# Kernel optimization log

Hardware: AMD Instinct MI355X
Metric: run time of the kernel (lower is better)

The kernel has to match this reference:

```python
import jax, jax.numpy as jnp
import numpy as np

B, S, DIN, H, N, L_S4, L_RES, ED = 512, 500, 14, 128, 256, 4, 6, 256


def setup_inputs() -> dict:
    key = jax.random.key(0)
    ks = jax.random.split(key, 32)
    f = jnp.float32
    rn = lambda k, sh, s: jax.random.normal(k, sh, f) * s
    inp = {
        'x': rn(ks[0], (B, S, DIN), 1.0),
        'timesteps': jax.random.randint(ks[1], (B,), 0, 1000),
        'mask': (jax.random.uniform(ks[2], (B, S, 1)) < 0.9).astype(f),
        'observed': rn(ks[3], (B, S, DIN), 1.0),
        'W_in': rn(ks[4], (DIN, H), DIN ** -0.5), 'b_in': jnp.zeros((H,), f),
        'time_W1': rn(ks[5], (ED, 2 * H), ED ** -0.5), 'time_b1': jnp.zeros((2 * H,), f),
        'time_W2': rn(ks[6], (2 * H, H), (2 * H) ** -0.5), 'time_b2': jnp.zeros((H,), f),
        's4_ln_g': jnp.ones((L_S4, H), f), 's4_ln_b': jnp.zeros((L_S4, H), f),
        's4_logA': jnp.log(0.5 * jnp.ones((L_S4, H, N), f)),
        's4_Aim': jnp.broadcast_to(np.pi * jnp.arange(N, dtype=f), (L_S4, H, N)).copy(),
        's4_Cre': rn(ks[7], (L_S4, H, N), 0.5 ** 0.5),
        's4_Cim': rn(ks[8], (L_S4, H, N), 0.5 ** 0.5),
        's4_D': rn(ks[9], (L_S4, H), 1.0),
        's4_logdt': jax.random.uniform(ks[10], (L_S4, H), f, np.log(0.001), np.log(0.1)),
        's4_Wo': rn(ks[11], (L_S4, H, H), H ** -0.5), 's4_bo': jnp.zeros((L_S4, H), f),
        'res_ln_g': jnp.ones((L_RES, H), f), 'res_ln_b': jnp.zeros((L_RES, H), f),
        'res_W1': rn(ks[12], (L_RES, H, 2 * H), H ** -0.5), 'res_b1': jnp.zeros((L_RES, 2 * H), f),
        'res_W2': rn(ks[13], (L_RES, 2 * H, H), (2 * H) ** -0.5), 'res_b2': jnp.zeros((L_RES, H), f),
        'W_out': rn(ks[14], (H, DIN), H ** -0.5), 'b_out': jnp.zeros((DIN,), f),
    }
    return inp


def _ln(x, g, b):
    m = x.mean(-1, keepdims=True)
    v = ((x - m) ** 2).mean(-1, keepdims=True)
    return (x - m) * jax.lax.rsqrt(v + 1e-5) * g + b


def reference(x, timesteps, mask, observed, W_in, b_in, time_W1, time_b1, time_W2,
              time_b2, s4_ln_g, s4_ln_b, s4_logA, s4_Aim, s4_Cre, s4_Cim, s4_D,
              s4_logdt, s4_Wo, s4_bo, res_ln_g, res_ln_b, res_W1, res_b1, res_W2,
              res_b2, W_out, b_out):
    Bb, Ss, _ = x.shape
    Hh = W_in.shape[1]
    x_cond = x * mask + observed
    # sinusoidal positional encoding gated by mask -> [B,S,H]
    pos = jnp.arange(Ss, dtype=jnp.float32)
    div = jnp.exp(-jnp.log(10000.0) * 2.0 * jnp.arange(Hh // 2, dtype=jnp.float32) / Hh)
    ang = pos[:, None] * div
    pe = jnp.concatenate([jnp.sin(ang), jnp.cos(ang)], -1)  # [S,H]
    h = x_cond @ W_in + b_in + pe[None] * mask
    # S4D layers: prenorm -> FFT causal conv with Vandermonde kernel -> GELU -> proj -> residual
    t_idx = jnp.arange(Ss, dtype=jnp.float32)
    for l in range(s4_logA.shape[0]):
        z = _ln(h, s4_ln_g[l], s4_ln_b[l])
        dt = jnp.exp(s4_logdt[l])[:, None]                       # [H,1]
        A = -jnp.exp(s4_logA[l]) + 1j * s4_Aim[l]                # [H,N]
        dtA = dt * A
        C = (s4_Cre[l] + 1j * s4_Cim[l]) * (jnp.exp(dtA) - 1.0) / A
        V = jnp.exp(dtA[:, :, None] * t_idx)                     # [H,N,S]
        K = 2.0 * jnp.einsum('hn,hnl->hl', C, V).real            # [H,S]
        u = jnp.transpose(z, (0, 2, 1))                          # [B,H,S]
        n = 2 * Ss
        y = jnp.fft.irfft(jnp.fft.rfft(u, n) * jnp.fft.rfft(K, n), n)[..., :Ss]
        y = y + s4_D[l][None, :, None] * u
        y = jax.nn.gelu(jnp.transpose(y, (0, 2, 1)), approximate=False)
        h = h + y @ s4_Wo[l] + s4_bo[l]
    # diffusion time embedding
    half = time_W1.shape[0] // 2
    emb = jnp.log(10000.0) / (half - 1)
    freqs = jnp.exp(-emb * jnp.arange(half, dtype=jnp.float32))
    te = timesteps.astype(jnp.float32)[:, None] * freqs
    te = jnp.concatenate([jnp.sin(te), jnp.cos(te)], -1)
    te = jax.nn.silu(te @ time_W1 + time_b1) @ time_W2 + time_b2
    h = h + te[:, None, :]
    # residual MLP blocks
    for l in range(res_W1.shape[0]):
        z = _ln(h, res_ln_g[l], res_ln_b[l])
        h = h + jax.nn.gelu(z @ res_W1[l] + res_b1[l], approximate=False) @ res_W2[l] + res_b2[l]
    return h @ W_out + b_out
```

## Files before the change

### kernel.cpp

```cpp
#include <hip/hip_runtime.h>
#include <math.h>

#define B_ 512
#define S_ 500
#define SP_ 512
#define DIN_ 14
#define H_ 128
#define N_ 256
#define NT_ 256000

#define SWZ(r) ((((r) ^ ((r) >> 4)) & 15) << 4)

typedef __attribute__((ext_vector_type(8))) short short8v;
typedef __attribute__((ext_vector_type(4))) short short4v;
typedef __attribute__((ext_vector_type(4))) float f32x4;

__device__ __forceinline__ float gelu_f(float x) {
    float e = __expf(-1.702f * x);
    return __fdividef(x, 1.0f + e);
}
__device__ __forceinline__ short f2bf(float f) {
    unsigned u = __builtin_bit_cast(unsigned, f);
    u += 0x7fffu + ((u >> 16) & 1u);
    return (short)(u >> 16);
}
__device__ __forceinline__ float bf2f(short s) {
    return __builtin_bit_cast(float, ((unsigned)(unsigned short)s) << 16);
}

__global__ __launch_bounds__(256) void k_kmat(
    const float* __restrict__ logA, const float* __restrict__ Aim,
    const float* __restrict__ Cre, const float* __restrict__ Cim,
    const float* __restrict__ logdt, float* __restrict__ Km)
{
    int lh = blockIdx.x;
    __shared__ float sCr[256], sCi[256], sAr[256], sAif[256];
    {
        int n = threadIdx.x;
        int idx = lh * N_ + n;
        double dt  = exp((double)logdt[lh]);
        double Are = -exp((double)logA[idx]);
        double Aiv = (double)Aim[idx];
        double ar  = dt * Are, ai = dt * Aiv;
        double er  = exp(ar);
        double E1r = er * cos(ai) - 1.0, E1i = er * sin(ai);
        double inv = 1.0 / (Are * Are + Aiv * Aiv);
        double qR  = (E1r * Are + E1i * Aiv) * inv;
        double qI  = (E1i * Are - E1r * Aiv) * inv;
        double cre = (double)Cre[idx], cim = (double)Cim[idx];
        sCr[n] = (float)(cre * qR - cim * qI);
        sCi[n] = (float)(cre * qI + cim * qR);
        sAr[n] = (float)ar;
        sAif[n] = (float)fmod(ai, 6.283185307179586476925286766559);
    }
    __syncthreads();
    for (int s = threadIdx.x; s < SP_; s += 256) {
        float acc = 0.0f;
        if (s < S_) {
            float fs = (float)s;
            for (int n = 0; n < N_; ++n) {
                float er = __expf(sAr[n] * fs);
                float y = sAif[n] * fs;
                y -= 6.28318530717958648f * rintf(y * 0.159154943091895336f);
                float sn, cs; __sincosf(y, &sn, &cs);
// ... 51 lines not shown
        float m = mask[tok];
        float a0 = b0, a1 = b1;
        const float* xp = x + (size_t)tok * DIN_;
        const float* op = obs + (size_t)tok * DIN_;
#pragma unroll
        for (int d = 0; d < DIN_; ++d) {
            float xc = xp[d] * m + op[d];
            a0 += xc * w0[d];
            a1 += xc * w1[d];
        }
        float h0 = a0 + pet[s * 128 + lane] * m;
        float h1 = a1 + pet[s * 128 + lane + 64] * m;
        float s1 = h0 + h1, s2 = h0 * h0 + h1 * h1;
#pragma unroll
        for (int off = 32; off > 0; off >>= 1) {
            s1 += __shfl_xor(s1, off, 64);
            s2 += __shfl_xor(s2, off, 64);
        }
        float mu = s1 * 0.0078125f;
        float rs = rsqrtf(s2 * 0.0078125f - mu * mu + 1e-5f);
        if (lane == 0) st[tok] = make_float2(mu, rs);
        h[(size_t)tok * H_ + lane] = h0;
        h[(size_t)tok * H_ + lane + 64] = h1;
    }
}

__global__ __launch_bounds__(256) void k_temb(
    const int* __restrict__ ts, const float* __restrict__ W1,
    const float* __restrict__ b1, const float* __restrict__ W2,
    const float* __restrict__ b2, float* __restrict__ te)
{
    __shared__ float feat[256];
    __shared__ float mid[256];
    int b = blockIdx.x, j = threadIdx.x;
    float t = (float)ts[b];
    float fr = expf(-0.07252236513367075f * (float)(j & 127));
    float ang = t * fr;
    feat[j] = (j < 128) ? sinf(ang) : cosf(ang);
    __syncthreads();
    float acc = b1[j];
    for (int k = 0; k < 256; ++k) acc += feat[k] * W1[k * 256 + j];
    mid[j] = acc / (1.0f + expf(-acc));
    __syncthreads();
    if (j < 128) {
        float a2 = b2[j];
        for (int k = 0; k < 256; ++k) a2 += mid[k] * W2[k * 128 + j];
        te[b * 128 + j] = a2;
    }
}

__global__ __launch_bounds__(256) void k_wcast(
    const float* __restrict__ Wo, const float* __restrict__ rW1,
    const float* __restrict__ rW2,
    short* __restrict__ WoT, short* __restrict__ W1T, short* __restrict__ W2T)
{
    int i = blockIdx.x * 256 + threadIdx.x;
    if (i < 65536) {
        int l = i >> 14, r = i & 16383, n = r >> 7, k = r & 127;
        WoT[i] = f2bf(Wo[(size_t)(l * 128 + k) * 128 + n]);
    } else if (i < 262144) {
        int j = i - 65536;
        int l = j >> 15, r = j & 32767, n = r >> 7, k = r & 127;
        W1T[j] = f2bf(rW1[(size_t)(l * 128 + k) * 256 + n]);
    } else if (i < 458752) {
        int j = i - 262144;
        int l = j >> 15, r = j & 32767, n = r >> 8, k = r & 255;
        W2T[j] = f2bf(rW2[(size_t)(l * 256 + k) * 128 + n]);
    }
}

__global__ __launch_bounds__(256) void k_ln_tb(
    const float* __restrict__ h, const float2* __restrict__ stc,
    const float* __restrict__ g, const float* __restrict__ be,
    short* __restrict__ ubt)
{
    int b = blockIdx.x, s0 = blockIdx.y * 64;
    int ntok = min(64, S_ - s0);
    __shared__ float tile[64 * 129];
    __shared__ float mu_[64], rs_[64];
    for (int idx = threadIdx.x; idx < (ntok << 7); idx += 256) {
        int i = idx >> 7, k = idx & 127;
        tile[i * 129 + k] = h[(size_t)(b * S_ + s0 + i) * H_ + k];
    }
    if (threadIdx.x < ntok) {
        float2 ms = stc[(size_t)b * S_ + s0 + threadIdx.x];
        mu_[threadIdx.x] = ms.x; rs_[threadIdx.x] = ms.y;
    }
    __syncthreads();
    for (int idx = threadIdx.x; idx < 128 * 32; idx += 256) {
        int k = idx >> 5, i = (idx & 31) * 2;
        float v0 = (i < ntok)     ? (tile[i * 129 + k]       - mu_[i])     * rs_[i]     * g[k] + be[k] : 0.f;
        float v1 = (i + 1 < ntok) ? (tile[(i + 1) * 129 + k] - mu_[i + 1]) * rs_[i + 1] * g[k] + be[k] : 0.f;
        unsigned lo = (unsigned short)f2bf(v0);
        unsigned hi = (unsigned short)f2bf(v1);
        *(unsigned*)(ubt + ((size_t)b * H_ + k) * SP_ + s0 + i) = lo | (hi << 16);
    }
}

__global__ __launch_bounds__(256) void k_cgemm(
    const short* __restrict__ ubt, const short* __restrict__ Tblk,
    const float* __restrict__ D, short* __restrict__ ybt)
{
    __shared__ short As[16384];
    __shared__ short Bs[16384];
    int hh = blockIdx.x, si = blockIdx.y, bt = blockIdx.z;
    int tid = threadIdx.x;
    int lane = tid & 63, wid = tid >> 6;
    int wm = wid >> 1, wn = wid & 1;
    int fr = lane & 15, ko = (lane >> 4) << 3;
    const short* Ab = ubt + ((size_t)(bt * 128) * H_ + hh) * SP_;

    f32x4 acc[4][4];
    f32x4 zv = {0.f, 0.f, 0.f, 0.f};
#pragma unroll
    for (int m = 0; m < 4; ++m)
#pragma unroll
        for (int n = 0; n < 4; ++n) acc[m][n] = zv;

    for (int tj = 0; tj <= si; ++tj) {
        if (tj) __syncthreads();
// ... 143 lines not shown
                }
                acc[m][n][j] = v;
                s1 += v; s2 += v * v;
            }
            s1 += __shfl_xor(s1, 1, 64); s2 += __shfl_xor(s2, 1, 64);
            s1 += __shfl_xor(s1, 2, 64); s2 += __shfl_xor(s2, 2, 64);
            s1 += __shfl_xor(s1, 4, 64); s2 += __shfl_xor(s2, 4, 64);
            s1 += __shfl_xor(s1, 8, 64); s2 += __shfl_xor(s2, 8, 64);
            if (fr == 0) {
                red[(wn * 128 + rl) * 2]     = s1;
                red[(wn * 128 + rl) * 2 + 1] = s2;
            }
        }
    }
    __syncthreads();
#pragma unroll
    for (int m = 0; m < 4; ++m) {
#pragma unroll
        for (int j = 0; j < 4; ++j) {
            int rl = wm * 64 + m * 16 + (lane >> 4) * 4 + j;
            int R = bm * 128 + rl;
            int b_ = R >> 9, s = R & 511;
            bool valid = (s < S_);
            float s1 = red[rl * 2]     + red[(128 + rl) * 2];
            float s2 = red[rl * 2 + 1] + red[(128 + rl) * 2 + 1];
            float mu = s1 * 0.0078125f;
            float rs = rsqrtf(s2 * 0.0078125f - mu * mu + 1e-5f);
            if (valid && fr == 0 && wn == 0)
                st[(size_t)b_ * S_ + s] = make_float2(mu, rs);
            if (un) {
#pragma unroll
                for (int n = 0; n < 4; ++n) {
                    int C = wn * 64 + n * 16 + fr;
                    float z = valid ? (acc[m][n][j] - mu) * rs * gn[C] + bn[C] : 0.f;
                    *(short*)((char*)znT + C * 256 + ((rl * 2) ^ SWZ(C))) = f2bf(z);
                }
            }
        }
    }
    if (un) {
        __syncthreads();
#pragma unroll
        for (int p = 0; p < 8; ++p) {
            int idx = p * 256 + tid;
            int C = idx >> 4, rlg = idx & 15;
            short8v z8 = *(const short8v*)((const char*)znT + C * 256 + ((rlg * 16) ^ SWZ(C)));
            *(short8v*)(un + (((size_t)(bl * 128 + C)) << 9) + s0t + rlg * 8) = z8;
        }
    }
}

__global__ __launch_bounds__(512) void k_mlp(
    float* hres, const float2* __restrict__ st,
    const short* __restrict__ W1T, const float* __restrict__ rb1,
    const short* __restrict__ W2T, const float* __restrict__ rb2,
    const float* __restrict__ g6, const float* __restrict__ b6)
{
    __shared__ __align__(16) char As1[32768];
    __shared__ __align__(16) char BsA[32768];
    int tid = threadIdx.x;
    int lane = tid & 63, wid = tid >> 6;
    int tq = wid >> 1, cq = wid & 1;
    int fr = lane & 15, q = lane >> 4;
    int ko = q * 8, q4 = q * 4;
    size_t tok0 = (size_t)blockIdx.x * 128;

    f32x4 v[4][2];
    f32x4 zvv = {0.f, 0.f, 0.f, 0.f};

#pragma unroll
    for (int nn = 0; nn < 2; ++nn) {
        int tok = tq * 32 + nn * 16 + fr;
        float2 ms = st[tok0 + tok];
        const float* hp = hres + (tok0 + tok) * 128;
#pragma unroll
        for (int m2 = 0; m2 < 4; ++m2) {
            int cb = m2 * 32 + cq * 16 + q4;
            float4 hv = *(const float4*)(hp + cb);
            v[m2][nn][0] = hv.x; v[m2][nn][1] = hv.y;
            v[m2][nn][2] = hv.z; v[m2][nn][3] = hv.w;
            float4 gv = *(const float4*)(g6 + cb);
            float4 bv = *(const float4*)(b6 + cb);
            short4v z;
            z[0] = f2bf((hv.x - ms.x) * ms.y * gv.x + bv.x);
            z[1] = f2bf((hv.y - ms.x) * ms.y * gv.y + bv.y);
            z[2] = f2bf((hv.z - ms.x) * ms.y * gv.z + bv.z);
            z[3] = f2bf((hv.w - ms.x) * ms.y * gv.w + bv.w);
            *(short4v*)(As1 + tok * 256 + ((cb * 2) ^ SWZ(tok))) = z;
        }
    }

    for (int l = 0; l < 6; ++l) {
        const short* W1 = W1T + l * 32768;
        const short* W2 = W2T + l * 32768;

        f32x4 acc1[2][4][2];
#pragma unroll
        for (int gy = 0; gy < 2; ++gy)
#pragma unroll
            for (int m1 = 0; m1 < 4; ++m1)
#pragma unroll
                for (int nn = 0; nn < 2; ++nn) acc1[gy][m1][nn] = zvv;

#pragma unroll
        for (int gy = 0; gy < 2; ++gy) {
#pragma unroll
            for (int p = 0; p < 4; ++p) {
                int idx = p * 512 + tid;
                int row = idx >> 4, c16 = idx & 15;
                int byt = row * 256 + ((c16 * 16) ^ SWZ(row));
                *(short8v*)(BsA + byt) =
                    *(const short8v*)(W1 + (size_t)(gy * 128 + row) * 128 + c16 * 8);
            }
            __syncthreads();
#pragma unroll
            for (int ks = 0; ks < 4; ++ks) {
                short8v b[2];
#pragma unroll
                for (int nn = 0; nn < 2; ++nn) {
                    int row = tq * 32 + nn * 16 + fr;
                    b[nn] = *(const short8v*)(As1 + row * 256 + (((ks * 32 + ko) * 2) ^ SWZ(row)));
                }
#pragma unroll
                for (int m1 = 0; m1 < 4; ++m1) {
                    int row = m1 * 32 + cq * 16 + fr;
                    short8v a = *(const short8v*)(BsA + row * 256 + (((ks * 32 + ko) * 2) ^ SWZ(row)));
#pragma unroll
                    for (int nn = 0; nn < 2; ++nn)
                        acc1[gy][m1][nn] = __builtin_amdgcn_mfma_f32_16x16x32_bf16(
                            a, b[nn], acc1[gy][m1][nn], 0, 0, 0);
                }
            }
            __syncthreads();
        }

        f32x4 acc2[4][2];
#pragma unroll
        for (int m2 = 0; m2 < 4; ++m2)
#pragma unroll
            for (int nn = 0; nn < 2; ++nn) acc2[m2][nn] = zvv;
#pragma unroll
        for (int kk = 0; kk < 2; ++kk) {
#pragma unroll
            for (int m1 = 0; m1 < 4; ++m1) {
                int nb = m1 * 32 + cq * 16 + q4;
                float4 bv = *(const float4*)(rb1 + l * 256 + kk * 128 + nb);
#pragma unroll
                for (int nn = 0; nn < 2; ++nn) {
                    int tok = tq * 32 + nn * 16 + fr;
                    short4v mz;
                    mz[0] = f2bf(gelu_f(acc1[kk][m1][nn][0] + bv.x));
                    mz[1] = f2bf(gelu_f(acc1[kk][m1][nn][1] + bv.y));
                    mz[2] = f2bf(gelu_f(acc1[kk][m1][nn][2] + bv.z));
                    mz[3] = f2bf(gelu_f(acc1[kk][m1][nn][3] + bv.w));
                    *(short4v*)(As1 + tok * 256 + ((nb * 2) ^ SWZ(tok))) = mz;
                }
            }
#pragma unroll
            for (int p = 0; p < 4; ++p) {
                int idx = p * 512 + tid;
                int row = idx >> 4, c16 = idx & 15;
                int byt = row * 256 + ((c16 * 16) ^ SWZ(row));
                *(short8v*)(BsA + byt) =
                    *(const short8v*)(W2 + (size_t)row * 256 + kk * 128 + c16 * 8);
            }
            __syncthreads();
#pragma unroll
            for (int ks = 0; ks < 4; ++ks) {
                short8v b[2];
#pragma unroll
                for (int nn = 0; nn < 2; ++nn) {
                    int row = tq * 32 + nn * 16 + fr;
                    b[nn] = *(const short8v*)(As1 + row * 256 + (((ks * 32 + ko) * 2) ^ SWZ(row)));
                }
#pragma unroll
                for (int m2 = 0; m2 < 4; ++m2) {
                    int row = m2 * 32 + cq * 16 + fr;
                    short8v a = *(const short8v*)(BsA + row * 256 + (((ks * 32 + ko) * 2) ^ SWZ(row)));
#pragma unroll
                    for (int nn = 0; nn < 2; ++nn)
                        acc2[m2][nn] = __builtin_amdgcn_mfma_f32_16x16x32_bf16(
                            a, b[nn], acc2[m2][nn], 0, 0, 0);
                }
            }
            __syncthreads();
        }

#pragma unroll
        for (int m2 = 0; m2 < 4; ++m2) {
            int cb = m2 * 32 + cq * 16 + q4;
            float4 b2v = *(const float4*)(rb2 + l * 128 + cb);
#pragma unroll
            for (int nn = 0; nn < 2; ++nn) {
                v[m2][nn][0] += acc2[m2][nn][0] + b2v.x;
                v[m2][nn][1] += acc2[m2][nn][1] + b2v.y;
                v[m2][nn][2] += acc2[m2][nn][2] + b2v.z;
                v[m2][nn][3] += acc2[m2][nn][3] + b2v.w;
            }
        }
        if (l < 5) {
            float* red = (float*)BsA;
            float s1[2] = {0.f, 0.f}, s2[2] = {0.f, 0.f};
#pragma unroll
            for (int nn = 0; nn < 2; ++nn) {
#pragma unroll
                for (int m2 = 0; m2 < 4; ++m2)
#pragma unroll
                    for (int j = 0; j < 4; ++j) {
                        float t = v[m2][nn][j];
                        s1[nn] += t; s2[nn] += t * t;
                    }
                s1[nn] += __shfl_xor(s1[nn], 16, 64);
                s1[nn] += __shfl_xor(s1[nn], 32, 64);
                s2[nn] += __shfl_xor(s2[nn], 16, 64);
                s2[nn] += __shfl_xor(s2[nn], 32, 64);
                if (q == 0) {
                    int tok = tq * 32 + nn * 16 + fr;
                    red[tok * 2 + cq] = s1[nn];
                    red[256 + tok * 2 + cq] = s2[nn];
                }
            }
            __syncthreads();
            const float* gl = g6 + (l + 1) * 128;
            const float* bl2 = b6 + (l + 1) * 128;
#pragma unroll
            for (int nn = 0; nn < 2; ++nn) {
                int tok = tq * 32 + nn * 16 + fr;
                float S1 = red[tok * 2] + red[tok * 2 + 1];
                float S2 = red[256 + tok * 2] + red[256 + tok * 2 + 1];
                float mu = S1 * 0.0078125f;
                float rs = rsqrtf(S2 * 0.0078125f - mu * mu + 1e-5f);
#pragma unroll
                for (int m2 = 0; m2 < 4; ++m2) {
                    int cb = m2 * 32 + cq * 16 + q4;
                    float4 gv = *(const float4*)(gl + cb);
                    float4 bv = *(const float4*)(bl2 + cb);
                    short4v z;
                    z[0] = f2bf((v[m2][nn][0] - mu) * rs * gv.x + bv.x);
                    z[1] = f2bf((v[m2][nn][1] - mu) * rs * gv.y + bv.y);
                    z[2] = f2bf((v[m2][nn][2] - mu) * rs * gv.z + bv.z);
                    z[3] = f2bf((v[m2][nn][3] - mu) * rs * gv.w + bv.w);
                    *(short4v*)(As1 + tok * 256 + ((cb * 2) ^ SWZ(tok))) = z;
                }
            }
            __syncthreads();
        }
    }

#pragma unroll
    for (int nn = 0; nn < 2; ++nn) {
        int tok = tq * 32 + nn * 16 + fr;
        float* hp = hres + (tok0 + tok) * 128;
#pragma unroll
        for (int m2 = 0; m2 < 4; ++m2) {
            int cb = m2 * 32 + cq * 16 + q4;
            float4 o;
            o.x = v[m2][nn][0]; o.y = v[m2][nn][1];
            o.z = v[m2][nn][2]; o.w = v[m2][nn][3];
            *(float4*)(hp + cb) = o;
        }
    }
}

__global__ __launch_bounds__(256) void k_out(
    const float* __restrict__ h, const float* __restrict__ Wout,
    const float* __restrict__ bout, float* __restrict__ out)
{
    __shared__ float wt[16 * 132];
    __shared__ float tile[64 * 132];
    int tok0 = blockIdx.x * 64;
    for (int idx = threadIdx.x; idx < 2048; idx += 256) {
        int j = idx >> 7, k = idx & 127;
        wt[j * 132 + k] = (j < 14) ? Wout[k * 14 + j] : 0.f;
    }
    const float4* hp = (const float4*)(h + (size_t)tok0 * 128);
    for (int idx = threadIdx.x; idx < 2048; idx += 256) {
        int row = idx >> 5, c4 = idx & 31;
        *((float4*)(tile + row * 132) + c4) = hp[idx];
    }
    __syncthreads();
    int i = threadIdx.x >> 2, jq = threadIdx.x & 3;
    float aj[4] = {0.f, 0.f, 0.f, 0.f};
    const float4* tr = (const float4*)(tile + i * 132);
#pragma unroll 8
    for (int kk = 0; kk < 32; ++kk) {
        float4 hv = tr[kk];
#pragma unroll
        for (int r = 0; r < 4; ++r) {
            float4 wv = *((const float4*)(wt + (jq * 4 + r) * 132) + kk);
            aj[r] += hv.x * wv.x + hv.y * wv.y + hv.z * wv.z + hv.w * wv.w;
        }
    }
#pragma unroll
    for (int r = 0; r < 4; ++r) {
        int j = jq * 4 + r;
        if (j < 14)
            out[(size_t)(tok0 + i) * 14 + j] = aj[r] + bout[j];
    }
}

extern "C" void kernel_launch(void* const* d_in, const int* in_sizes, int n_in,
                              void* d_out, int out_size, void* d_ws, size_t ws_size,
                              hipStream_t stream)
{
    (void)in_sizes; (void)n_in; (void)out_size;
    const float* x      = (const float*)d_in[0];
    const int*   tsteps = (const int*)  d_in[1];
    const float* mask   = (const float*)d_in[2];
    const float* obs    = (const float*)d_in[3];
    const float* Win    = (const float*)d_in[4];
    const float* bin    = (const float*)d_in[5];
    const float* tW1    = (const float*)d_in[6];
    const float* tb1    = (const float*)d_in[7];
    const float* tW2    = (const float*)d_in[8];
    const float* tb2    = (const float*)d_in[9];
    const float* lng4   = (const float*)d_in[10];
    const float* lnb4   = (const float*)d_in[11];
    const float* logA   = (const float*)d_in[12];
    const float* Aim    = (const float*)d_in[13];
    const float* Cre    = (const float*)d_in[14];
    const float* Cim    = (const float*)d_in[15];
    const float* Dp     = (const float*)d_in[16];
    const float* logdt  = (const float*)d_in[17];
    const float* Wo     = (const float*)d_in[18];
    const float* bo     = (const float*)d_in[19];
    const float* lng6   = (const float*)d_in[20];
    const float* lnb6   = (const float*)d_in[21];
    const float* rW1    = (const float*)d_in[22];
    const float* rb1    = (const float*)d_in[23];
    const float* rW2    = (const float*)d_in[24];
    const float* rb2    = (const float*)d_in[25];
    const float* Woutp  = (const float*)d_in[26];
    const float* boutp  = (const float*)d_in[27];

    float*  ws  = (float*)d_ws;
    float*  h   = ws;
    float*  Km  = h + 32768000;
    float*  te  = Km + 262144;
    float2* st  = (float2*)(te + 65536);
    float*  pet = (float*)st + 512000;
    short*  WoT = (short*)(pet + 64000);
    short*  W1T = WoT + 65536;
    short*  W2T = W1T + 196608;
    float*  big = (float*)(W2T + 196608);
    size_t  wf  = ws_size / sizeof(float);
    size_t  fixed = 33901056;
    size_t  avail = (wf > fixed) ? (wf - fixed) : 0;

    bool flowA = (avail >= 29360128);

    k_kmat<<<512, 256, 0, stream>>>(logA, Aim, Cre, Cim, logdt, Km);
    k_petab<<<S_, 128, 0, stream>>>(pet);
    k_inproj<<<NT_ / 16, 256, 0, stream>>>(x, mask, obs, Win, bin, pet, h, st);
    k_temb<<<B_, 256, 0, stream>>>(tsteps, tW1, tb1, tW2, tb2, te);
    k_wcast<<<1792, 256, 0, stream>>>(Wo, rW1, rW2, WoT, W1T, W2T);

    if (flowA) {
        short* ubtA = (short*)big;
        short* ubtB = ubtA + 16777216;
        short* ybt  = ubtB + 16777216;
        short* Tblk = ybt + 16777216;

        k_ln_tb<<<dim3(256, 8), 256, 0, stream>>>(h, st, lng4, lnb4, ubtA);
        k_ln_tb<<<dim3(256, 8), 256, 0, stream>>>(
            h + (size_t)256 * S_ * H_, st + (size_t)256 * S_, lng4, lnb4, ubtB);

        for (int l = 0; l < 4; ++l) {
            k_toep<<<dim3(H_, 4), 256, 0, stream>>>(Km + (size_t)l * H_ * SP_, Tblk);
            for (int cb = 0; cb < 2; ++cb) {
                size_t bOff = (size_t)cb * 256;
                float* hb = h + bOff * S_ * H_;
                short* ub = cb ? ubtB : ubtA;
                const float* tep = (l == 3) ? (te + bOff * H_) : (const float*)0;
                short* un = (l < 3) ? ub : (short*)0;
                k_cgemm<<<dim3(H_, 4, 2), 256, 0, stream>>>(ub, Tblk, Dp + l * H_, ybt);
                k_p4<<<1024, 256, 0, stream>>>(
                    ybt, WoT + l * 16384, bo + l * H_, tep, hb, st + bOff * S_,
                    un, lng4 + (l + 1) * H_, lnb4 + (l + 1) * H_);
            }
        }
    } else {
        int CHB = 64;
        for (int c = 256; c >= 64; c >>= 1)
            if ((size_t)c * 65536 + 4194304 <= avail) { CHB = c; break; }
        short* ubt  = (short*)big;
        short* ybt  = ubt + (size_t)CHB * 65536;
        short* Tblk = ybt + (size_t)CHB * 65536;
        int nCB = B_ / CHB;
        for (int l = 0; l < 4; ++l) {
            k_toep<<<dim3(H_, 4), 256, 0, stream>>>(Km + (size_t)l * H_ * SP_, Tblk);
            for (int cb = 0; cb < nCB; ++cb) {
                size_t bOff = (size_t)cb * CHB;
                float* hb = h + bOff * S_ * H_;
                const float* tep = (l == 3) ? (te + bOff * H_) : (const float*)0;
                k_ln_tb<<<dim3(CHB, 8), 256, 0, stream>>>(
                    hb, st + bOff * S_, lng4 + l * H_, lnb4 + l * H_, ubt);
                k_cgemm<<<dim3(H_, 4, CHB / 128), 256, 0, stream>>>(
                    ubt, Tblk, Dp + l * H_, ybt);
                k_p4<<<CHB * 4, 256, 0, stream>>>(
                    ybt, WoT + l * 16384, bo + l * H_, tep, hb, st + bOff * S_,
                    (short*)0, lng4, lnb4);
            }
        }
    }

    k_mlp<<<NT_ / 128, 512, 0, stream>>>(h, st, W1T, rb1, W2T, rb2, lng6, lnb6);

    k_out<<<NT_ / 64, 256, 0, stream>>>(h, Woutp, boutp, (float*)d_out);
}
```

Baseline: 2.003 ms.

## Restructure residual MLP kernel with pre-swizzled weight images and register double-buffered prefetch

The weight-cast kernel now writes the MLP weights into one pre-swizzled bf16 image, split into four 128x128 chunks per layer. This lets the MLP kernel copy each chunk straight into shared memory without recomputing addresses. The MLP kernel now has each wave own 16 full-width tokens, so the LayerNorm row reduction uses only shuffles and no longer needs a shared-memory exchange and barrier. Each weight chunk is prefetched into registers one stage ahead and stored into separate ping-pong LDS buffers, which removes one barrier per stage. In exchange, LDS use per block doubles to 128KB and register pressure rises, which may lower occupancy.

```diff
diff --git a/kernel.cpp b/kernel.cpp
--- a/kernel.cpp
+++ b/kernel.cpp
@@ -167,20 +167,27 @@
 __global__ __launch_bounds__(256) void k_wcast(
     const float* __restrict__ Wo, const float* __restrict__ rW1,
     const float* __restrict__ rW2,
-    short* __restrict__ WoT, short* __restrict__ W1T, short* __restrict__ W2T)
+    short* __restrict__ WoT, short* __restrict__ Wimg)
 {
     int i = blockIdx.x * 256 + threadIdx.x;
     if (i < 65536) {
         int l = i >> 14, r = i & 16383, n = r >> 7, k = r & 127;
         WoT[i] = f2bf(Wo[(size_t)(l * 128 + k) * 128 + n]);
-    } else if (i < 262144) {
+    } else {
         int j = i - 65536;
-        int l = j >> 15, r = j & 32767, n = r >> 7, k = r & 127;
-        W1T[j] = f2bf(rW1[(size_t)(l * 128 + k) * 256 + n]);
-    } else if (i < 458752) {
-        int j = i - 262144;
-        int l = j >> 15, r = j & 32767, n = r >> 8, k = r & 255;
-        W2T[j] = f2bf(rW2[(size_t)(l * 256 + k) * 128 + n]);
+        int l = j >> 16;
+        int r = j & 65535;
+        int which = r >> 14;
+        int d = r & 16383;
+        int row = d >> 7, off = d & 127;
+        int c16 = (off >> 3) ^ ((row ^ (row >> 4)) & 15);
+        int k = c16 * 8 + (off & 7);
+        float val;
+        if (which == 0)      val = rW1[(size_t)(l * 128 + k) * 256 + row];
+        else if (which == 1) val = rW1[(size_t)(l * 128 + k) * 256 + 128 + row];
+        else if (which == 2) val = rW2[(size_t)(l * 256 + k) * 128 + row];
+        else                 val = rW2[(size_t)(l * 256 + 128 + k) * 128 + row];
+        Wimg[j] = f2bf(val);
     }
 }
 
@@ -430,33 +437,37 @@
 
 __global__ __launch_bounds__(512) void k_mlp(
     float* hres, const float2* __restrict__ st,
-    const short* __restrict__ W1T, const float* __restrict__ rb1,
-    const short* __restrict__ W2T, const float* __restrict__ rb2,
+    const short* __restrict__ Wimg, const float* __restrict__ rb1,
+    const float* __restrict__ rb2,
     const float* __restrict__ g6, const float* __restrict__ b6)
 {
-    __shared__ __align__(16) char As1[32768];
-    __shared__ __align__(16) char BsA[32768];
+    __shared__ __align__(16) char Zs[32768];
+    __shared__ __align__(16) char Ms[32768];
+    __shared__ __align__(16) char Wa[32768];
+    __shared__ __align__(16) char Wb[32768];
     int tid = threadIdx.x;
     int lane = tid & 63, wid = tid >> 6;
-    int tq = wid >> 1, cq = wid & 1;
     int fr = lane & 15, q = lane >> 4;
-    int ko = q * 8, q4 = q * 4;
+    int q4 = q * 4, ko = q * 8;
+    int trow = wid * 16 + fr;
     size_t tok0 = (size_t)blockIdx.x * 128;
 
-    f32x4 v[4][2];
-    f32x4 zvv = {0.f, 0.f, 0.f, 0.f};
-
-#pragma unroll
-    for (int nn = 0; nn < 2; ++nn) {
-        int tok = tq * 32 + nn * 16 + fr;
-        float2 ms = st[tok0 + tok];
-        const float* hp = hres + (tok0 + tok) * 128;
-#pragma unroll
-        for (int m2 = 0; m2 < 4; ++m2) {
-            int cb = m2 * 32 + cq * 16 + q4;
+    short8v tA[4], tB[4];
+    {
+        const short8v* gp = (const short8v*)Wimg;
+#pragma unroll
+        for (int p = 0; p < 4; ++p) tA[p] = gp[p * 512 + tid];
+    }
+
+    f32x4 v[8];
+    {
+        float2 ms = st[tok0 + trow];
+        const float* hp = hres + (tok0 + trow) * 128;
+#pragma unroll
+        for (int m = 0; m < 8; ++m) {
+            int cb = m * 16 + q4;
             float4 hv = *(const float4*)(hp + cb);
-            v[m2][nn][0] = hv.x; v[m2][nn][1] = hv.y;
-            v[m2][nn][2] = hv.z; v[m2][nn][3] = hv.w;
+            v[m][0] = hv.x; v[m][1] = hv.y; v[m][2] = hv.z; v[m][3] = hv.w;
             float4 gv = *(const float4*)(g6 + cb);
             float4 bv = *(const float4*)(b6 + cb);
             short4v z;
@@ -464,178 +475,175 @@
             z[1] = f2bf((hv.y - ms.x) * ms.y * gv.y + bv.y);
             z[2] = f2bf((hv.z - ms.x) * ms.y * gv.z + bv.z);
             z[3] = f2bf((hv.w - ms.x) * ms.y * gv.w + bv.w);
-            *(short4v*)(As1 + tok * 256 + ((cb * 2) ^ SWZ(tok))) = z;
-        }
-    }
-
+            *(short4v*)(Zs + trow * 256 + ((cb * 2) ^ SWZ(trow))) = z;
+        }
+    }
+#pragma unroll
+    for (int p = 0; p < 4; ++p) *(short8v*)(Wa + p * 8192 + tid * 16) = tA[p];
+    {
+        const short8v* gp = (const short8v*)(Wimg + 32768);
+#pragma unroll
+        for (int p = 0; p < 4; ++p) tB[p] = gp[p * 512 + tid];
+    }
+    __syncthreads();
+
+    f32x4 zvv = {0.f, 0.f, 0.f, 0.f};
     for (int l = 0; l < 6; ++l) {
-        const short* W1 = W1T + l * 32768;
-        const short* W2 = W2T + l * 32768;
-
-        f32x4 acc1[2][4][2];
-#pragma unroll
-        for (int gy = 0; gy < 2; ++gy)
-#pragma unroll
-            for (int m1 = 0; m1 < 4; ++m1)
-#pragma unroll
-                for (int nn = 0; nn < 2; ++nn) acc1[gy][m1][nn] = zvv;
-
-#pragma unroll
-        for (int gy = 0; gy < 2; ++gy) {
-#pragma unroll
-            for (int p = 0; p < 4; ++p) {
-                int idx = p * 512 + tid;
-                int row = idx >> 4, c16 = idx & 15;
-                int byt = row * 256 + ((c16 * 16) ^ SWZ(row));
-                *(short8v*)(BsA + byt) =
-                    *(const short8v*)(W1 + (size_t)(gy * 128 + row) * 128 + c16 * 8);
-            }
-            __syncthreads();
-#pragma unroll
-            for (int ks = 0; ks < 4; ++ks) {
-                short8v b[2];
-#pragma unroll
-                for (int nn = 0; nn < 2; ++nn) {
-                    int row = tq * 32 + nn * 16 + fr;
-                    b[nn] = *(const short8v*)(As1 + row * 256 + (((ks * 32 + ko) * 2) ^ SWZ(row)));
-                }
-#pragma unroll
-                for (int m1 = 0; m1 < 4; ++m1) {
-                    int row = m1 * 32 + cq * 16 + fr;
-                    short8v a = *(const short8v*)(BsA + row * 256 + (((ks * 32 + ko) * 2) ^ SWZ(row)));
-#pragma unroll
-                    for (int nn = 0; nn < 2; ++nn)
-                        acc1[gy][m1][nn] = __builtin_amdgcn_mfma_f32_16x16x32_bf16(
-                            a, b[nn], acc1[gy][m1][nn], 0, 0, 0);
-                }
-            }
-            __syncthreads();
-        }
-
-        f32x4 acc2[4][2];
-#pragma unroll
-        for (int m2 = 0; m2 < 4; ++m2)
-#pragma unroll
-            for (int nn = 0; nn < 2; ++nn) acc2[m2][nn] = zvv;
-#pragma unroll
-        for (int kk = 0; kk < 2; ++kk) {
-#pragma unroll
-            for (int m1 = 0; m1 < 4; ++m1) {
-                int nb = m1 * 32 + cq * 16 + q4;
-                float4 bv = *(const float4*)(rb1 + l * 256 + kk * 128 + nb);
-#pragma unroll
-                for (int nn = 0; nn < 2; ++nn) {
-                    int tok = tq * 32 + nn * 16 + fr;
-                    short4v mz;
-                    mz[0] = f2bf(gelu_f(acc1[kk][m1][nn][0] + bv.x));
-                    mz[1] = f2bf(gelu_f(acc1[kk][m1][nn][1] + bv.y));
-                    mz[2] = f2bf(gelu_f(acc1[kk][m1][nn][2] + bv.z));
-                    mz[3] = f2bf(gelu_f(acc1[kk][m1][nn][3] + bv.w));
-                    *(short4v*)(As1 + tok * 256 + ((nb * 2) ^ SWZ(tok))) = mz;
-                }
-            }
-#pragma unroll
-            for (int p = 0; p < 4; ++p) {
-                int idx = p * 512 + tid;
-                int row = idx >> 4, c16 = idx & 15;
-                int byt = row * 256 + ((c16 * 16) ^ SWZ(row));
-                *(short8v*)(BsA + byt) =
-                    *(const short8v*)(W2 + (size_t)row * 256 + kk * 128 + c16 * 8);
-            }
-            __syncthreads();
-#pragma unroll
-            for (int ks = 0; ks < 4; ++ks) {
-                short8v b[2];
-#pragma unroll
-                for (int nn = 0; nn < 2; ++nn) {
-                    int row = tq * 32 + nn * 16 + fr;
-                    b[nn] = *(const short8v*)(As1 + row * 256 + (((ks * 32 + ko) * 2) ^ SWZ(row)));
-                }
-#pragma unroll
-                for (int m2 = 0; m2 < 4; ++m2) {
-                    int row = m2 * 32 + cq * 16 + fr;
-                    short8v a = *(const short8v*)(BsA + row * 256 + (((ks * 32 + ko) * 2) ^ SWZ(row)));
-#pragma unroll
-                    for (int nn = 0; nn < 2; ++nn)
-                        acc2[m2][nn] = __builtin_amdgcn_mfma_f32_16x16x32_bf16(
-                            a, b[nn], acc2[m2][nn], 0, 0, 0);
-                }
-            }
-            __syncthreads();
-        }
-
-#pragma unroll
-        for (int m2 = 0; m2 < 4; ++m2) {
-            int cb = m2 * 32 + cq * 16 + q4;
+        const short* wl = Wimg + l * 65536;
+        f32x4 acc1[8], acc2[8];
+
+#pragma unroll
+        for (int m = 0; m < 8; ++m) acc1[m] = zvv;
+#pragma unroll
+        for (int ks = 0; ks < 4; ++ks) {
+            int kb = (ks * 32 + ko) * 2;
+            short8v bfr = *(const short8v*)(Zs + trow * 256 + (kb ^ SWZ(trow)));
+#pragma unroll
+            for (int m = 0; m < 8; ++m) {
+                int row = m * 16 + fr;
+                short8v afr = *(const short8v*)(Wa + row * 256 + (kb ^ SWZ(row)));
+                acc1[m] = __builtin_amdgcn_mfma_f32_16x16x32_bf16(afr, bfr, acc1[m], 0, 0, 0);
+            }
+        }
+#pragma unroll
+        for (int m = 0; m < 8; ++m) {
+            int cb = m * 16 + q4;
+            float4 bv = *(const float4*)(rb1 + l * 256 + cb);
+            short4v mz;
+            mz[0] = f2bf(gelu_f(acc1[m][0] + bv.x));
+            mz[1] = f2bf(gelu_f(acc1[m][1] + bv.y));
+            mz[2] = f2bf(gelu_f(acc1[m][2] + bv.z));
+            mz[3] = f2bf(gelu_f(acc1[m][3] + bv.w));
+            *(short4v*)(Ms + trow * 256 + ((cb * 2) ^ SWZ(trow))) = mz;
+        }
+#pragma unroll
+        for (int p = 0; p < 4; ++p) *(short8v*)(Wb + p * 8192 + tid * 16) = tB[p];
+        {
+            const short8v* gp = (const short8v*)(wl + 16384);
+#pragma unroll
+            for (int p = 0; p < 4; ++p) tA[p] = gp[p * 512 + tid];
+        }
+        __syncthreads();
+
+#pragma unroll
+        for (int m = 0; m < 8; ++m) acc2[m] = zvv;
+#pragma unroll
+        for (int ks = 0; ks < 4; ++ks) {
+            int kb = (ks * 32 + ko) * 2;
+            short8v bfr = *(const short8v*)(Ms + trow * 256 + (kb ^ SWZ(trow)));
+#pragma unroll
+            for (int m = 0; m < 8; ++m) {
+                int row = m * 16 + fr;
+                short8v afr = *(const short8v*)(Wb + row * 256 + (kb ^ SWZ(row)));
+                acc2[m] = __builtin_amdgcn_mfma_f32_16x16x32_bf16(afr, bfr, acc2[m], 0, 0, 0);
+            }
+        }
+#pragma unroll
+        for (int p = 0; p < 4; ++p) *(short8v*)(Wa + p * 8192 + tid * 16) = tA[p];
+        {
+            const short8v* gp = (const short8v*)(wl + 49152);
+#pragma unroll
+            for (int p = 0; p < 4; ++p) tB[p] = gp[p * 512 + tid];
+        }
+        __syncthreads();
+
+#pragma unroll
+        for (int m = 0; m < 8; ++m) acc1[m] = zvv;
+#pragma unroll
+        for (int ks = 0; ks < 4; ++ks) {
+            int kb = (ks * 32 + ko) * 2;
+            short8v bfr = *(const short8v*)(Zs + trow * 256 + (kb ^ SWZ(trow)));
+#pragma unroll
+            for (int m = 0; m < 8; ++m) {
+                int row = m * 16 + fr;
+                short8v afr = *(const short8v*)(Wa + row * 256 + (kb ^ SWZ(row)));
+                acc1[m] = __builtin_amdgcn_mfma_f32_16x16x32_bf16(afr, bfr, acc1[m], 0, 0, 0);
+            }
+        }
+#pragma unroll
+        for (int m = 0; m < 8; ++m) {
+            int cb = m * 16 + q4;
+            float4 bv = *(const float4*)(rb1 + l * 256 + 128 + cb);
+            short4v mz;
+            mz[0] = f2bf(gelu_f(acc1[m][0] + bv.x));
+            mz[1] = f2bf(gelu_f(acc1[m][1] + bv.y));
+            mz[2] = f2bf(gelu_f(acc1[m][2] + bv.z));
+            mz[3] = f2bf(gelu_f(acc1[m][3] + bv.w));
+            *(short4v*)(Ms + trow * 256 + ((cb * 2) ^ SWZ(trow))) = mz;
+        }
+#pragma unroll
+        for (int p = 0; p < 4; ++p) *(short8v*)(Wb + p * 8192 + tid * 16) = tB[p];
+        if (l < 5) {
+            const short8v* gp = (const short8v*)(wl + 65536);
+#pragma unroll
+            for (int p = 0; p < 4; ++p) tA[p] = gp[p * 512 + tid];
+        }
+        __syncthreads();
+
+#pragma unroll
+        for (int ks = 0; ks < 4; ++ks) {
+            int kb = (ks * 32 + ko) * 2;
+            short8v bfr = *(const short8v*)(Ms + trow * 256 + (kb ^ SWZ(trow)));
+#pragma unroll
+            for (int m = 0; m < 8; ++m) {
+                int row = m * 16 + fr;
+                short8v afr = *(const short8v*)(Wb + row * 256 + (kb ^ SWZ(row)));
+                acc2[m] = __builtin_amdgcn_mfma_f32_16x16x32_bf16(afr, bfr, acc2[m], 0, 0, 0);
+            }
+        }
+
+#pragma unroll
+        for (int m = 0; m < 8; ++m) {
+            int cb = m * 16 + q4;
             float4 b2v = *(const float4*)(rb2 + l * 128 + cb);
-#pragma unroll
-            for (int nn = 0; nn < 2; ++nn) {
-                v[m2][nn][0] += acc2[m2][nn][0] + b2v.x;
-                v[m2][nn][1] += acc2[m2][nn][1] + b2v.y;
-                v[m2][nn][2] += acc2[m2][nn][2] + b2v.z;
-                v[m2][nn][3] += acc2[m2][nn][3] + b2v.w;
-            }
+            v[m][0] += acc2[m][0] + b2v.x;
+            v[m][1] += acc2[m][1] + b2v.y;
+            v[m][2] += acc2[m][2] + b2v.z;
+            v[m][3] += acc2[m][3] + b2v.w;
         }
         if (l < 5) {
-            float* red = (float*)BsA;
-            float s1[2] = {0.f, 0.f}, s2[2] = {0.f, 0.f};
-#pragma unroll
-            for (int nn = 0; nn < 2; ++nn) {
-#pragma unroll
-                for (int m2 = 0; m2 < 4; ++m2)
-#pragma unroll
-                    for (int j = 0; j < 4; ++j) {
-                        float t = v[m2][nn][j];
-                        s1[nn] += t; s2[nn] += t * t;
-                    }
-                s1[nn] += __shfl_xor(s1[nn], 16, 64);
-                s1[nn] += __shfl_xor(s1[nn], 32, 64);
-                s2[nn] += __shfl_xor(s2[nn], 16, 64);
-                s2[nn] += __shfl_xor(s2[nn], 32, 64);
-                if (q == 0) {
-                    int tok = tq * 32 + nn * 16 + fr;
-                    red[tok * 2 + cq] = s1[nn];
-                    red[256 + tok * 2 + cq] = s2[nn];
-                }
-            }
-            __syncthreads();
+#pragma unroll
+            for (int p = 0; p < 4; ++p) *(short8v*)(Wa + p * 8192 + tid * 16) = tA[p];
+            float s1 = 0.f, s2 = 0.f;
+#pragma unroll
+            for (int m = 0; m < 8; ++m)
+#pragma unroll
+                for (int j = 0; j < 4; ++j) { float t = v[m][j]; s1 += t; s2 += t * t; }
+            s1 += __shfl_xor(s1, 16, 64); s2 += __shfl_xor(s2, 16, 64);
+            s1 += __shfl_xor(s1, 32, 64); s2 += __shfl_xor(s2, 32, 64);
+            float mu = s1 * 0.0078125f;
+            float rs = rsqrtf(s2 * 0.0078125f - mu * mu + 1e-5f);
+            {
+                const short8v* gp = (const short8v*)(wl + 65536 + 32768);
+#pragma unroll
+                for (int p = 0; p < 4; ++p) tB[p] = gp[p * 512 + tid];
+            }
             const float* gl = g6 + (l + 1) * 128;
             const float* bl2 = b6 + (l + 1) * 128;
 #pragma unroll
-            for (int nn = 0; nn < 2; ++nn) {
-                int tok = tq * 32 + nn * 16 + fr;
-                float S1 = red[tok * 2] + red[tok * 2 + 1];
-                float S2 = red[256 + tok * 2] + red[256 + tok * 2 + 1];
-                float mu = S1 * 0.0078125f;
-                float rs = rsqrtf(S2 * 0.0078125f - mu * mu + 1e-5f);
-#pragma unroll
-                for (int m2 = 0; m2 < 4; ++m2) {
-                    int cb = m2 * 32 + cq * 16 + q4;
-                    float4 gv = *(const float4*)(gl + cb);
-                    float4 bv = *(const float4*)(bl2 + cb);
-                    short4v z;
-                    z[0] = f2bf((v[m2][nn][0] - mu) * rs * gv.x + bv.x);
-                    z[1] = f2bf((v[m2][nn][1] - mu) * rs * gv.y + bv.y);
-                    z[2] = f2bf((v[m2][nn][2] - mu) * rs * gv.z + bv.z);
-                    z[3] = f2bf((v[m2][nn][3] - mu) * rs * gv.w + bv.w);
-                    *(short4v*)(As1 + tok * 256 + ((cb * 2) ^ SWZ(tok))) = z;
-                }
+            for (int m = 0; m < 8; ++m) {
+                int cb = m * 16 + q4;
+                float4 gv = *(const float4*)(gl + cb);
+                float4 bv = *(const float4*)(bl2 + cb);
+                short4v z;
+                z[0] = f2bf((v[m][0] - mu) * rs * gv.x + bv.x);
+                z[1] = f2bf((v[m][1] - mu) * rs * gv.y + bv.y);
+                z[2] = f2bf((v[m][2] - mu) * rs * gv.z + bv.z);
+                z[3] = f2bf((v[m][3] - mu) * rs * gv.w + bv.w);
+                *(short4v*)(Zs + trow * 256 + ((cb * 2) ^ SWZ(trow))) = z;
             }
             __syncthreads();
         }
     }
 
-#pragma unroll
-    for (int nn = 0; nn < 2; ++nn) {
-        int tok = tq * 32 + nn * 16 + fr;
-        float* hp = hres + (tok0 + tok) * 128;
-#pragma unroll
-        for (int m2 = 0; m2 < 4; ++m2) {
-            int cb = m2 * 32 + cq * 16 + q4;
+    {
+        float* hq = hres + (tok0 + trow) * 128;
+#pragma unroll
+        for (int m = 0; m < 8; ++m) {
+            int cb = m * 16 + q4;
             float4 o;
-            o.x = v[m2][nn][0]; o.y = v[m2][nn][1];
-            o.z = v[m2][nn][2]; o.w = v[m2][nn][3];
-            *(float4*)(hp + cb) = o;
+            o.x = v[m][0]; o.y = v[m][1]; o.z = v[m][2]; o.w = v[m][3];
+            *(float4*)(hq + cb) = o;
         }
     }
 }
@@ -711,17 +719,16 @@
     const float* Woutp  = (const float*)d_in[26];
     const float* boutp  = (const float*)d_in[27];
 
-    float*  ws  = (float*)d_ws;
-    float*  h   = ws;
-    float*  Km  = h + 32768000;
-    float*  te  = Km + 262144;
-    float2* st  = (float2*)(te + 65536);
-    float*  pet = (float*)st + 512000;
-    short*  WoT = (short*)(pet + 64000);
-    short*  W1T = WoT + 65536;
-    short*  W2T = W1T + 196608;
-    float*  big = (float*)(W2T + 196608);
-    size_t  wf  = ws_size / sizeof(float);
+    float*  ws   = (float*)d_ws;
+    float*  h    = ws;
+    float*  Km   = h + 32768000;
+    float*  te   = Km + 262144;
+    float2* st   = (float2*)(te + 65536);
+    float*  pet  = (float*)st + 512000;
+    short*  WoT  = (short*)(pet + 64000);
+    short*  Wimg = WoT + 65536;
+    float*  big  = (float*)(Wimg + 393216);
+    size_t  wf   = ws_size / sizeof(float);
     size_t  fixed = 33901056;
     size_t  avail = (wf > fixed) ? (wf - fixed) : 0;
 
@@ -731,7 +738,7 @@
     k_petab<<<S_, 128, 0, stream>>>(pet);
     k_inproj<<<NT_ / 16, 256, 0, stream>>>(x, mask, obs, Win, bin, pet, h, st);
     k_temb<<<B_, 256, 0, stream>>>(tsteps, tW1, tb1, tW2, tb2, te);
-    k_wcast<<<1792, 256, 0, stream>>>(Wo, rW1, rW2, WoT, W1T, W2T);
+    k_wcast<<<1792, 256, 0, stream>>>(Wo, rW1, rW2, WoT, Wimg);
 
     if (flowA) {
         short* ubtA = (short*)big;
@@ -782,7 +789,7 @@
         }
     }
 
-    k_mlp<<<NT_ / 128, 512, 0, stream>>>(h, st, W1T, rb1, W2T, rb2, lng6, lnb6);
+    k_mlp<<<NT_ / 128, 512, 0, stream>>>(h, st, Wimg, rb1, rb2, lng6, lnb6);
 
     k_out<<<NT_ / 64, 256, 0, stream>>>(h, Woutp, boutp, (float*)d_out);
 }
```

Result: no change. 2.030 ms (+1.4%).

## Stage full MLP weight matrices in LDS and cut barriers in residual MLP kernel

Applied to the files above, without the earlier changes.

The residual MLP kernel now keeps the whole 256x128 W1 and 128x256 W2 matrices in 64KB LDS buffers and widens the activation buffer to 256 columns. Each GEMM then runs as a single pass over K, replacing the two half-K passes that each needed their own barriers. The next layer's W1 is loaded while the LayerNorm statistics reduction runs, overlapping the global loads with that work. This removes several __syncthreads per layer, at the cost of doubling LDS use to 128KB per block, which limits how many blocks fit on a CU.

```diff
diff --git a/kernel.cpp b/kernel.cpp
--- a/kernel.cpp
+++ b/kernel.cpp
@@ -10,6 +10,7 @@
 #define NT_ 256000
 
 #define SWZ(r) ((((r) ^ ((r) >> 4)) & 15) << 4)
+#define SWZ5(r) (((r) & 15) << 4)
 
 typedef __attribute__((ext_vector_type(8))) short short8v;
 typedef __attribute__((ext_vector_type(4))) short short4v;
@@ -434,8 +435,8 @@
     const short* __restrict__ W2T, const float* __restrict__ rb2,
     const float* __restrict__ g6, const float* __restrict__ b6)
 {
-    __shared__ __align__(16) char As1[32768];
-    __shared__ __align__(16) char BsA[32768];
+    __shared__ __align__(16) char As1[65536];
+    __shared__ __align__(16) char Ws[65536];
     int tid = threadIdx.x;
     int lane = tid & 63, wid = tid >> 6;
     int tq = wid >> 1, cq = wid & 1;
@@ -446,6 +447,13 @@
     f32x4 v[4][2];
     f32x4 zvv = {0.f, 0.f, 0.f, 0.f};
 
+#pragma unroll
+    for (int p = 0; p < 8; ++p) {
+        int idx = p * 512 + tid;
+        int row = idx >> 4, c16 = idx & 15;
+        *(short8v*)(Ws + row * 256 + ((c16 * 16) ^ SWZ(row))) =
+            *(const short8v*)(W1T + (size_t)row * 128 + c16 * 8);
+    }
 #pragma unroll
     for (int nn = 0; nn < 2; ++nn) {
         int tok = tq * 32 + nn * 16 + fr;
@@ -464,14 +472,12 @@
             z[1] = f2bf((hv.y - ms.x) * ms.y * gv.y + bv.y);
             z[2] = f2bf((hv.z - ms.x) * ms.y * gv.z + bv.z);
             z[3] = f2bf((hv.w - ms.x) * ms.y * gv.w + bv.w);
-            *(short4v*)(As1 + tok * 256 + ((cb * 2) ^ SWZ(tok))) = z;
-        }
-    }
+            *(short4v*)(As1 + tok * 512 + ((cb * 2) ^ SWZ5(tok))) = z;
+        }
+    }
+    __syncthreads();
 
     for (int l = 0; l < 6; ++l) {
-        const short* W1 = W1T + l * 32768;
-        const short* W2 = W2T + l * 32768;
-
         f32x4 acc1[2][4][2];
 #pragma unroll
         for (int gy = 0; gy < 2; ++gy)
@@ -479,90 +485,83 @@
             for (int m1 = 0; m1 < 4; ++m1)
 #pragma unroll
                 for (int nn = 0; nn < 2; ++nn) acc1[gy][m1][nn] = zvv;
-
-#pragma unroll
-        for (int gy = 0; gy < 2; ++gy) {
-#pragma unroll
-            for (int p = 0; p < 4; ++p) {
-                int idx = p * 512 + tid;
-                int row = idx >> 4, c16 = idx & 15;
-                int byt = row * 256 + ((c16 * 16) ^ SWZ(row));
-                *(short8v*)(BsA + byt) =
-                    *(const short8v*)(W1 + (size_t)(gy * 128 + row) * 128 + c16 * 8);
-            }
-            __syncthreads();
-#pragma unroll
-            for (int ks = 0; ks < 4; ++ks) {
-                short8v b[2];
-#pragma unroll
-                for (int nn = 0; nn < 2; ++nn) {
-                    int row = tq * 32 + nn * 16 + fr;
-                    b[nn] = *(const short8v*)(As1 + row * 256 + (((ks * 32 + ko) * 2) ^ SWZ(row)));
-                }
+#pragma unroll
+        for (int ks = 0; ks < 4; ++ks) {
+            int kb2 = (ks * 32 + ko) * 2;
+            short8v b[2];
+#pragma unroll
+            for (int nn = 0; nn < 2; ++nn) {
+                int row = tq * 32 + nn * 16 + fr;
+                b[nn] = *(const short8v*)(As1 + row * 512 + (kb2 ^ SWZ5(row)));
+            }
+#pragma unroll
+            for (int gy = 0; gy < 2; ++gy)
 #pragma unroll
                 for (int m1 = 0; m1 < 4; ++m1) {
-                    int row = m1 * 32 + cq * 16 + fr;
-                    short8v a = *(const short8v*)(BsA + row * 256 + (((ks * 32 + ko) * 2) ^ SWZ(row)));
+                    int row = gy * 128 + m1 * 32 + cq * 16 + fr;
+                    short8v a = *(const short8v*)(Ws + row * 256 + (kb2 ^ SWZ(row)));
 #pragma unroll
                     for (int nn = 0; nn < 2; ++nn)
                         acc1[gy][m1][nn] = __builtin_amdgcn_mfma_f32_16x16x32_bf16(
                             a, b[nn], acc1[gy][m1][nn], 0, 0, 0);
                 }
-            }
-            __syncthreads();
-        }
-
-        f32x4 acc2[4][2];
-#pragma unroll
-        for (int m2 = 0; m2 < 4; ++m2)
-#pragma unroll
-            for (int nn = 0; nn < 2; ++nn) acc2[m2][nn] = zvv;
-#pragma unroll
-        for (int kk = 0; kk < 2; ++kk) {
+        }
+        __syncthreads();
+
+#pragma unroll
+        for (int gy = 0; gy < 2; ++gy)
 #pragma unroll
             for (int m1 = 0; m1 < 4; ++m1) {
-                int nb = m1 * 32 + cq * 16 + q4;
-                float4 bv = *(const float4*)(rb1 + l * 256 + kk * 128 + nb);
+                int c = gy * 128 + m1 * 32 + cq * 16 + q4;
+                float4 bv = *(const float4*)(rb1 + l * 256 + c);
 #pragma unroll
                 for (int nn = 0; nn < 2; ++nn) {
                     int tok = tq * 32 + nn * 16 + fr;
                     short4v mz;
-                    mz[0] = f2bf(gelu_f(acc1[kk][m1][nn][0] + bv.x));
-                    mz[1] = f2bf(gelu_f(acc1[kk][m1][nn][1] + bv.y));
-                    mz[2] = f2bf(gelu_f(acc1[kk][m1][nn][2] + bv.z));
-                    mz[3] = f2bf(gelu_f(acc1[kk][m1][nn][3] + bv.w));
-                    *(short4v*)(As1 + tok * 256 + ((nb * 2) ^ SWZ(tok))) = mz;
+                    mz[0] = f2bf(gelu_f(acc1[gy][m1][nn][0] + bv.x));
+                    mz[1] = f2bf(gelu_f(acc1[gy][m1][nn][1] + bv.y));
+                    mz[2] = f2bf(gelu_f(acc1[gy][m1][nn][2] + bv.z));
+                    mz[3] = f2bf(gelu_f(acc1[gy][m1][nn][3] + bv.w));
+                    *(short4v*)(As1 + tok * 512 + ((c * 2) ^ SWZ5(tok))) = mz;
                 }
             }
-#pragma unroll
-            for (int p = 0; p < 4; ++p) {
+        {
+            const short* W2 = W2T + l * 32768;
+#pragma unroll
+            for (int p = 0; p < 8; ++p) {
                 int idx = p * 512 + tid;
-                int row = idx >> 4, c16 = idx & 15;
-                int byt = row * 256 + ((c16 * 16) ^ SWZ(row));
-                *(short8v*)(BsA + byt) =
-                    *(const short8v*)(W2 + (size_t)row * 256 + kk * 128 + c16 * 8);
-            }
-            __syncthreads();
-#pragma unroll
-            for (int ks = 0; ks < 4; ++ks) {
-                short8v b[2];
-#pragma unroll
-                for (int nn = 0; nn < 2; ++nn) {
-                    int row = tq * 32 + nn * 16 + fr;
-                    b[nn] = *(const short8v*)(As1 + row * 256 + (((ks * 32 + ko) * 2) ^ SWZ(row)));
-                }
-#pragma unroll
-                for (int m2 = 0; m2 < 4; ++m2) {
-                    int row = m2 * 32 + cq * 16 + fr;
-                    short8v a = *(const short8v*)(BsA + row * 256 + (((ks * 32 + ko) * 2) ^ SWZ(row)));
-#pragma unroll
-                    for (int nn = 0; nn < 2; ++nn)
-                        acc2[m2][nn] = __builtin_amdgcn_mfma_f32_16x16x32_bf16(
-                            a, b[nn], acc2[m2][nn], 0, 0, 0);
-                }
-            }
-            __syncthreads();
-        }
+                int row = idx >> 5, c16 = idx & 31;
+                *(short8v*)(Ws + row * 512 + ((c16 * 16) ^ SWZ5(row))) =
+                    *(const short8v*)(W2 + (size_t)row * 256 + c16 * 8);
+            }
+        }
+        __syncthreads();
+
+        f32x4 acc2[4][2];
+#pragma unroll
+        for (int m2 = 0; m2 < 4; ++m2)
+#pragma unroll
+            for (int nn = 0; nn < 2; ++nn) acc2[m2][nn] = zvv;
+#pragma unroll
+        for (int ks = 0; ks < 8; ++ks) {
+            int kb2 = (ks * 32 + ko) * 2;
+            short8v b[2];
+#pragma unroll
+            for (int nn = 0; nn < 2; ++nn) {
+                int row = tq * 32 + nn * 16 + fr;
+                b[nn] = *(const short8v*)(As1 + row * 512 + (kb2 ^ SWZ5(row)));
+            }
+#pragma unroll
+            for (int m2 = 0; m2 < 4; ++m2) {
+                int row = m2 * 32 + cq * 16 + fr;
+                short8v a = *(const short8v*)(Ws + row * 512 + (kb2 ^ SWZ5(row)));
+#pragma unroll
+                for (int nn = 0; nn < 2; ++nn)
+                    acc2[m2][nn] = __builtin_amdgcn_mfma_f32_16x16x32_bf16(
+                        a, b[nn], acc2[m2][nn], 0, 0, 0);
+            }
+        }
+        __syncthreads();
 
 #pragma unroll
         for (int m2 = 0; m2 < 4; ++m2) {
@@ -577,7 +576,15 @@
             }
         }
         if (l < 5) {
-            float* red = (float*)BsA;
+            const short* W1n = W1T + (l + 1) * 32768;
+#pragma unroll
+            for (int p = 0; p < 8; ++p) {
+                int idx = p * 512 + tid;
+                int row = idx >> 4, c16 = idx & 15;
+                *(short8v*)(Ws + row * 256 + ((c16 * 16) ^ SWZ(row))) =
+                    *(const short8v*)(W1n + (size_t)row * 128 + c16 * 8);
+            }
+            float* red = (float*)As1;
             float s1[2] = {0.f, 0.f}, s2[2] = {0.f, 0.f};
 #pragma unroll
             for (int nn = 0; nn < 2; ++nn) {
@@ -592,33 +599,42 @@
                 s1[nn] += __shfl_xor(s1[nn], 32, 64);
                 s2[nn] += __shfl_xor(s2[nn], 16, 64);
                 s2[nn] += __shfl_xor(s2[nn], 32, 64);
-                if (q == 0) {
+            }
+            if (q == 0) {
+#pragma unroll
+                for (int nn = 0; nn < 2; ++nn) {
                     int tok = tq * 32 + nn * 16 + fr;
                     red[tok * 2 + cq] = s1[nn];
                     red[256 + tok * 2 + cq] = s2[nn];
                 }
             }
             __syncthreads();
-            const float* gl = g6 + (l + 1) * 128;
-            const float* bl2 = b6 + (l + 1) * 128;
+            float mu2[2], rs2[2];
 #pragma unroll
             for (int nn = 0; nn < 2; ++nn) {
                 int tok = tq * 32 + nn * 16 + fr;
                 float S1 = red[tok * 2] + red[tok * 2 + 1];
                 float S2 = red[256 + tok * 2] + red[256 + tok * 2 + 1];
-                float mu = S1 * 0.0078125f;
-                float rs = rsqrtf(S2 * 0.0078125f - mu * mu + 1e-5f);
+                mu2[nn] = S1 * 0.0078125f;
+                rs2[nn] = rsqrtf(S2 * 0.0078125f - mu2[nn] * mu2[nn] + 1e-5f);
+            }
+            __syncthreads();
+            const float* gl = g6 + (l + 1) * 128;
+            const float* bl2 = b6 + (l + 1) * 128;
+#pragma unroll
+            for (int nn = 0; nn < 2; ++nn) {
+                int tok = tq * 32 + nn * 16 + fr;
 #pragma unroll
                 for (int m2 = 0; m2 < 4; ++m2) {
                     int cb = m2 * 32 + cq * 16 + q4;
                     float4 gv = *(const float4*)(gl + cb);
                     float4 bv = *(const float4*)(bl2 + cb);
                     short4v z;
-                    z[0] = f2bf((v[m2][nn][0] - mu) * rs * gv.x + bv.x);
-                    z[1] = f2bf((v[m2][nn][1] - mu) * rs * gv.y + bv.y);
-                    z[2] = f2bf((v[m2][nn][2] - mu) * rs * gv.z + bv.z);
-                    z[3] = f2bf((v[m2][nn][3] - mu) * rs * gv.w + bv.w);
-                    *(short4v*)(As1 + tok * 256 + ((cb * 2) ^ SWZ(tok))) = z;
+                    z[0] = f2bf((v[m2][nn][0] - mu2[nn]) * rs2[nn] * gv.x + bv.x);
+                    z[1] = f2bf((v[m2][nn][1] - mu2[nn]) * rs2[nn] * gv.y + bv.y);
+                    z[2] = f2bf((v[m2][nn][2] - mu2[nn]) * rs2[nn] * gv.z + bv.z);
+                    z[3] = f2bf((v[m2][nn][3] - mu2[nn]) * rs2[nn] * gv.w + bv.w);
+                    *(short4v*)(As1 + tok * 512 + ((cb * 2) ^ SWZ5(tok))) = z;
                 }
             }
             __syncthreads();
```

After: 2.056 ms. 1.03x slower.
